# Kernel optimization log

Hardware: AMD Instinct MI355X
Metric: run time of the kernel (lower is better)

## Reference

```python
import jax, jax.numpy as jnp
import numpy as np

D_MODEL = 1024
N_HEADS = 16
D_K = D_MODEL // N_HEADS


def _glorot(key, fan_in, fan_out):
    limit = np.sqrt(6.0 / (fan_in + fan_out)).astype(np.float32)
    return jax.random.uniform(key, (fan_in, fan_out), jnp.float32, -limit, limit)


def setup_inputs() -> dict:
    key = jax.random.key(0)
    kx, kq, kk, kv = jax.random.split(key, 4)
    x = jax.random.normal(kx, (2, 2048, D_MODEL), jnp.float32)
    Wq = _glorot(kq, D_MODEL, D_MODEL)
    Wk = _glorot(kk, D_MODEL, D_MODEL)
    Wv = _glorot(kv, D_MODEL, D_MODEL)
    bq = jnp.zeros((D_MODEL,), jnp.float32)
    bk = jnp.zeros((D_MODEL,), jnp.float32)
    bv = jnp.zeros((D_MODEL,), jnp.float32)
    return {"x": x, "Wq": Wq, "bq": bq, "Wk": Wk, "bk": bk, "Wv": Wv, "bv": bv}


def reference(x, Wq, bq, Wk, bk, Wv, bv):
    B, S, _ = x.shape
    # QKV projections (Dense layers with bias)
    q = (x @ Wq + bq).reshape(B, S, N_HEADS, D_K).transpose(0, 2, 1, 3)  # [B,H,S,Dk]
    k = (x @ Wk + bk).reshape(B, S, N_HEADS, D_K).transpose(0, 2, 1, 3)
    v = (x @ Wv + bv).reshape(B, S, N_HEADS, D_K).transpose(0, 2, 1, 3)
    # raw exp-based softmax (NO max subtraction, per original module)
    scores = jnp.einsum('bhqd,bhkd->bhqk', q, k) / np.sqrt(D_K).astype(np.float32)
    scores = jnp.exp(scores)
    attn = scores / (jnp.sum(scores, axis=-1, keepdims=True) + 1e-8)
    context = jnp.einsum('bhqk,bhkd->bhqd', attn, v)  # [B,H,S,Dk]
    return context.transpose(0, 2, 1, 3).reshape(B, S, N_HEADS * D_K)
```

## Files before the change

### kernel.cpp

```cpp
#include <hip/hip_runtime.h>
#include <hip/hip_bf16.h>
#include <stdint.h>

typedef __bf16 bf16x8 __attribute__((ext_vector_type(8)));
typedef __bf16 bf16x4 __attribute__((ext_vector_type(4)));
typedef float  f32x4  __attribute__((ext_vector_type(4)));
typedef unsigned short u16_t;

#define MFMA(a, b, c) __builtin_amdgcn_mfma_f32_16x16x32_bf16((a), (b), (c), 0, 0, 0)

__device__ __forceinline__ void cp16(const void* g, void* l) {
  __builtin_amdgcn_global_load_lds(
      (const __attribute__((address_space(1))) unsigned int*)g,
      (__attribute__((address_space(3))) unsigned int*)l, 16, 0, 0);
}

__device__ __forceinline__ unsigned pkbf(float a, float b) {
  __bf16 x = (__bf16)a, y = (__bf16)b;
  return ((unsigned)*(u16_t*)&y << 16) | (unsigned)*(u16_t*)&x;
}

__global__ __launch_bounds__(256) void k_cvt_x(const float* __restrict__ in,
                                               u16_t* __restrict__ out, int n4) {
  int i = blockIdx.x * 256 + threadIdx.x;
  if (i >= n4) return;
  float4 f = ((const float4*)in)[i];
  bf16x4 o = {(__bf16)f.x, (__bf16)f.y, (__bf16)f.z, (__bf16)f.w};
  *(bf16x4*)&out[(size_t)i * 4] = o;
}

__global__ __launch_bounds__(256) void k_cvt_w(const float* __restrict__ W0,
                                               const float* __restrict__ W1,
                                               const float* __restrict__ W2,
                                               u16_t* __restrict__ Wt) {
  __shared__ u16_t T[64][65];
  const float* W = blockIdx.z == 0 ? W0 : (blockIdx.z == 1 ? W1 : W2);
  int k0 = blockIdx.y * 64, n0 = blockIdx.x * 64;
  int t = threadIdx.x;
#pragma unroll
  for (int i = 0; i < 16; i++) {
    int e = i * 256 + t, r = e >> 6, c = e & 63;
    __bf16 hv = (__bf16)W[(size_t)(k0 + r) * 1024 + n0 + c];
    T[r][c] = *(u16_t*)&hv;
  }
  __syncthreads();
  size_t base = ((size_t)blockIdx.z * 1024 + n0) * 1024 + k0;
#pragma unroll
  for (int i = 0; i < 16; i++) {
    int e = i * 256 + t, r = e >> 6, c = e & 63;
    Wt[base + (size_t)r * 1024 + c] = T[c][r];
  }
}

__global__ __launch_bounds__(256) void k_gemm_qkv(
    const u16_t* __restrict__ A, const u16_t* __restrict__ Bt,
    const float* __restrict__ bq, const float* __restrict__ bk,
    const float* __restrict__ bv,
    u16_t* __restrict__ Qo, u16_t* __restrict__ Ko, u16_t* __restrict__ Vo) {
  __shared__ u16_t As[128 * 32];
  __shared__ u16_t Bs[128 * 32];
  const int tid = threadIdx.x, lane = tid & 63, wv = tid >> 6;
  const int quad = lane >> 4, col = lane & 15;
  const int wm = wv >> 1, wn = wv & 1;
  const int tn = blockIdx.x * 128, tm = blockIdx.y * 128;
  f32x4 acc[4][4] = {};

  const int c0 = wv * 2;
  const int srow = lane >> 2;
  const int spc = lane & 3;

  for (int kk = 0; kk < 1024; kk += 32) {
#pragma unroll
    for (int i = 0; i < 2; i++) {
      int c = c0 + i;
      int m = c * 16 + srow;
      int lch = spc ^ ((m >> 1) & 3);
      cp16(A + (size_t)(tm + m) * 1024 + kk + lch * 8, As + c * 512 + lane * 8);
      cp16(Bt + (size_t)(tn + m) * 1024 + kk + lch * 8, Bs + c * 512 + lane * 8);
    }
    __syncthreads();
    bf16x8 af[4], bfv[4];
#pragma unroll
    for (int mt = 0; mt < 4; mt++) {
      int row = wm * 64 + mt * 16 + col;
      af[mt] = *(const bf16x8*)&As[row * 32 + (quad ^ ((row >> 1) & 3)) * 8];
    }
#pragma unroll
    for (int nt = 0; nt < 4; nt++) {
      int row = wn * 64 + nt * 16 + col;
      bfv[nt] = *(const bf16x8*)&Bs[row * 32 + (quad ^ ((row >> 1) & 3)) * 8];
    }
#pragma unroll
    for (int mt = 0; mt < 4; mt++)
#pragma unroll
      for (int nt = 0; nt < 4; nt++)
        acc[mt][nt] = MFMA(af[mt], bfv[nt], acc[mt][nt]);
    __syncthreads();
  }

  const int mat = tn >> 10;
  const float* bias = mat == 0 ? bq : (mat == 1 ? bk : bv);
  if (mat == 2) {
#pragma unroll
    for (int nt = 0; nt < 4; nt++) {
      int gn = tn + wn * 64 + nt * 16 + col;
      int d = gn & 1023, h = d >> 6, dk = d & 63;
      float bb = bias[d];
#pragma unroll
      for (int mt = 0; mt < 4; mt++) {
        int gm = tm + wm * 64 + mt * 16 + quad * 4;
        int b = gm >> 11, s = gm & 2047;
        bf16x4 pk4;
#pragma unroll
        for (int r = 0; r < 4; r++) pk4[r] = (__bf16)(acc[mt][nt][r] + bb);
        *(bf16x4*)&Vo[((size_t)((b * 16 + h) * 64 + dk)) * 2048 + s] = pk4;
      }
    }
  } else {
    u16_t* O = mat == 0 ? Qo : Ko;
    const float scl = mat == 0 ? 0.18033688011112042f : 1.0f;
#pragma unroll
    for (int nt = 0; nt < 4; nt++) {
      int gn = tn + wn * 64 + nt * 16 + col;
      int d = gn & 1023, h = d >> 6, dk = d & 63;
      float bb = bias[d];
#pragma unroll
      for (int mt = 0; mt < 4; mt++) {
#pragma unroll
        for (int r = 0; r < 4; r++) {
          int gm = tm + wm * 64 + mt * 16 + quad * 4 + r;
          int b = gm >> 11, s = gm & 2047;
          __bf16 hv = (__bf16)((acc[mt][nt][r] + bb) * scl);
          O[((size_t)((b * 16 + h) * 2048 + s)) * 64 + dk] = *(u16_t*)&hv;
        }
      }
    }
  }
}

__global__ __launch_bounds__(128, 2) void k_attn(const u16_t* __restrict__ Q,
                                                 const u16_t* __restrict__ K,
                                                 const u16_t* __restrict__ Vt,
                                                 float* __restrict__ out) {
  __shared__ u16_t smem[20480];
  u16_t* Qs  = smem;
  u16_t* Ksb = smem + 4096;
  u16_t* Vsb = smem + 12288;
  const int tid = threadIdx.x, lane = tid & 63, wk = tid >> 6;
  const int quad = lane >> 4, col = lane & 15;
  const int qt = blockIdx.x, bh = blockIdx.y;
  const int b = bh >> 4, h = bh & 15;
  const int r8 = lane >> 3, c8 = lane & 7;

  const u16_t* Qg = Q + ((size_t)bh * 2048 + qt * 64) * 64;
  const u16_t* Kg = K + (size_t)bh * 2048 * 64;
  const u16_t* Vg = Vt + (size_t)bh * 64 * 2048;

#pragma unroll
  for (int i = 0; i < 4; i++) {
    int c = wk * 4 + i;
    int row = c * 8 + r8;
    int lch = c8 ^ (row & 7);
    cp16(Qg + (size_t)row * 64 + lch * 8, Qs + c * 512 + lane * 8);
    cp16(Kg + (size_t)row * 64 + lch * 8, Ksb + c * 512 + lane * 8);
    cp16(Vg + (size_t)row * 2048 + lch * 8, Vsb + c * 512 + lane * 8);
  }
  __syncthreads();

  bf16x8 qf[4][2];
#pragma unroll
  for (int nt = 0; nt < 4; nt++)
#pragma unroll
    for (int ks = 0; ks < 2; ks++) {
      int row = nt * 16 + col;
      qf[nt][ks] = *(const bf16x8*)&Qs[row * 64 + (((ks * 4 + quad) ^ (row & 7)) * 8)];
    }
  __syncthreads();

  u16_t* Pw = Qs + wk * 2048;

  bf16x8 ones;
#pragma unroll
  for (int j = 0; j < 8; j++) ones[j] = (__bf16)1.0f;

  f32x4 ao[4][4] = {};
  f32x4 dn[4] = {};

  for (int kt = 0; kt < 32; kt++) {
    const int cur = kt & 1;
    const u16_t* Kc = Ksb + cur * 4096;
    const u16_t* Vc = Vsb + cur * 4096;
    if (kt + 1 < 32) {
      u16_t* Kn = Ksb + (cur ^ 1) * 4096;
      u16_t* Vn = Vsb + (cur ^ 1) * 4096;
#pragma unroll
      for (int i = 0; i < 4; i++) {
        int c = wk * 4 + i;
        int row = c * 8 + r8;
        int lch = c8 ^ (row & 7);
        cp16(Kg + (size_t)(kt + 1) * 4096 + (size_t)row * 64 + lch * 8,
             Kn + c * 512 + lane * 8);
        cp16(Vg + (size_t)row * 2048 + (kt + 1) * 64 + lch * 8,
             Vn + c * 512 + lane * 8);
      }
    }

    f32x4 sc[2][4] = {};
#pragma unroll
    for (int ks = 0; ks < 2; ks++) {
      bf16x8 kf[2];
#pragma unroll
      for (int mt = 0; mt < 2; mt++) {
        int row = wk * 32 + mt * 16 + col;
        kf[mt] = *(const bf16x8*)&Kc[row * 64 + (((ks * 4 + quad) ^ (row & 7)) * 8)];
      }
#pragma unroll
      for (int mt = 0; mt < 2; mt++)
#pragma unroll
        for (int nt = 0; nt < 4; nt++)
          sc[mt][nt] = MFMA(kf[mt], qf[nt][ks], sc[mt][nt]);
    }

#pragma unroll
    for (int mt = 0; mt < 2; mt++)
#pragma unroll
      for (int nt = 0; nt < 4; nt++) {
        int ql = nt * 16 + col;
        unsigned lo = pkbf(__builtin_amdgcn_exp2f(sc[mt][nt][0]),
                           __builtin_amdgcn_exp2f(sc[mt][nt][1]));
        unsigned hi = pkbf(__builtin_amdgcn_exp2f(sc[mt][nt][2]),
                           __builtin_amdgcn_exp2f(sc[mt][nt][3]));
        int kp = (mt * 16 + quad * 4) ^ (((ql >> 1) & 3) << 3);
        *(uint2*)&Pw[ql * 32 + kp] = make_uint2(lo, hi);
      }

    bf16x8 vf[4];
#pragma unroll
    for (int dt = 0; dt < 4; dt++) {
      int row = dt * 16 + col;
      vf[dt] = *(const bf16x8*)&Vc[row * 64 + (((wk * 4 + quad) ^ (row & 7)) * 8)];
    }

#pragma unroll
    for (int nt = 0; nt < 4; nt++) {
      int ql = nt * 16 + col;
      bf16x8 pf = *(const bf16x8*)&Pw[ql * 32 + ((quad * 8) ^ (((ql >> 1) & 3) << 3))];
      dn[nt] = MFMA(pf, ones, dn[nt]);
#pragma unroll
      for (int dt = 0; dt < 4; dt++)
        ao[nt][dt] = MFMA(pf, vf[dt], ao[nt][dt]);
    }
    __syncthreads();
  }

  float* red = (float*)(smem + 4096);
  if (wk == 1) {
#pragma unroll
    for (int nt = 0; nt < 4; nt++) {
#pragma unroll
      for (int dt = 0; dt < 4; dt++)
#pragma unroll
        for (int r = 0; r < 4; r++)
          red[lane * 81 + (nt * 4 + dt) * 4 + r] = ao[nt][dt][r];
#pragma unroll
      for (int r = 0; r < 4; r++)
        red[lane * 81 + 64 + nt * 4 + r] = dn[nt][r];
    }
  }
  __syncthreads();
  if (wk == 0) {
#pragma unroll
    for (int nt = 0; nt < 4; nt++) {
      float dsum[4];
#pragma unroll
      for (int r = 0; r < 4; r++)
        dsum[r] = dn[nt][r] + red[lane * 81 + 64 + nt * 4 + r] + 1e-8f;
#pragma unroll
      for (int dt = 0; dt < 4; dt++) {
#pragma unroll
        for (int r = 0; r < 4; r++) {
          float v = (ao[nt][dt][r] + red[lane * 81 + (nt * 4 + dt) * 4 + r]) / dsum[r];
          int s = qt * 64 + nt * 16 + quad * 4 + r;
          out[((size_t)b * 2048 + s) * 1024 + h * 64 + dt * 16 + col] = v;
        }
      }
    }
  }
}

extern "C" void kernel_launch(void* const* d_in, const int* in_sizes, int n_in,
                              void* d_out, int out_size, void* d_ws, size_t ws_size,
                              hipStream_t stream) {
  const float* x  = (const float*)d_in[0];
  const float* Wq = (const float*)d_in[1];
  const float* bq = (const float*)d_in[2];
  const float* Wk = (const float*)d_in[3];
  const float* bk = (const float*)d_in[4];
  const float* Wv = (const float*)d_in[5];
  const float* bv = (const float*)d_in[6];
  float* out = (float*)d_out;

  char* ws = (char*)d_ws;
  u16_t* xb  = (u16_t*)(ws);
  u16_t* Wt  = (u16_t*)(ws + 8388608);
  u16_t* Qb  = (u16_t*)(ws + 14680064);
  u16_t* Kb  = (u16_t*)(ws + 23068672);
  u16_t* Vtb = (u16_t*)(ws + 31457280);

  hipLaunchKernelGGL(k_cvt_x, dim3(4096), dim3(256), 0, stream, x, xb, 1048576);
  hipLaunchKernelGGL(k_cvt_w, dim3(16, 16, 3), dim3(256), 0, stream, Wq, Wk, Wv, Wt);
  hipLaunchKernelGGL(k_gemm_qkv, dim3(24, 32), dim3(256), 0, stream,
                     xb, Wt, bq, bk, bv, Qb, Kb, Vtb);
  hipLaunchKernelGGL(k_attn, dim3(32, 32), dim3(128), 0, stream, Qb, Kb, Vtb, out);
}
```

Baseline: 172.1 us.

## Split attention block into four waves over query and key halves; merge prep kernels

The attention kernel moves from 2 waves to 4 waves per block. Each wave now handles half the query rows and half of each key tile, and the P-tile layout and the cross-wave reduction are adapted to match. The intent is to cut per-wave register pressure and raise occupancy and latency hiding. The x conversion and weight transpose kernels are fused into one launch to save a kernel launch. In exchange there is more LDS traffic and synchronization per block, with more waves contending for the same shared tiles.

```diff
diff --git a/kernel.cpp b/kernel.cpp
--- a/kernel.cpp
+++ b/kernel.cpp
@@ -20,23 +20,25 @@
   return ((unsigned)*(u16_t*)&y << 16) | (unsigned)*(u16_t*)&x;
 }
 
-__global__ __launch_bounds__(256) void k_cvt_x(const float* __restrict__ in,
-                                               u16_t* __restrict__ out, int n4) {
-  int i = blockIdx.x * 256 + threadIdx.x;
-  if (i >= n4) return;
-  float4 f = ((const float4*)in)[i];
-  bf16x4 o = {(__bf16)f.x, (__bf16)f.y, (__bf16)f.z, (__bf16)f.w};
-  *(bf16x4*)&out[(size_t)i * 4] = o;
-}
-
-__global__ __launch_bounds__(256) void k_cvt_w(const float* __restrict__ W0,
-                                               const float* __restrict__ W1,
-                                               const float* __restrict__ W2,
-                                               u16_t* __restrict__ Wt) {
+__global__ __launch_bounds__(256) void k_prep(const float* __restrict__ x,
+                                              const float* __restrict__ W0,
+                                              const float* __restrict__ W1,
+                                              const float* __restrict__ W2,
+                                              u16_t* __restrict__ xb,
+                                              u16_t* __restrict__ Wt) {
   __shared__ u16_t T[64][65];
-  const float* W = blockIdx.z == 0 ? W0 : (blockIdx.z == 1 ? W1 : W2);
-  int k0 = blockIdx.y * 64, n0 = blockIdx.x * 64;
-  int t = threadIdx.x;
+  int bx = blockIdx.x, t = threadIdx.x;
+  if (bx < 4096) {
+    int i = bx * 256 + t;
+    float4 f = ((const float4*)x)[i];
+    bf16x4 o = {(__bf16)f.x, (__bf16)f.y, (__bf16)f.z, (__bf16)f.w};
+    *(bf16x4*)&xb[(size_t)i * 4] = o;
+    return;
+  }
+  int j = bx - 4096;
+  int nx = j & 15, ny = (j >> 4) & 15, z = j >> 8;
+  const float* W = z == 0 ? W0 : (z == 1 ? W1 : W2);
+  int k0 = ny * 64, n0 = nx * 64;
 #pragma unroll
   for (int i = 0; i < 16; i++) {
     int e = i * 256 + t, r = e >> 6, c = e & 63;
@@ -44,7 +46,7 @@
     T[r][c] = *(u16_t*)&hv;
   }
   __syncthreads();
-  size_t base = ((size_t)blockIdx.z * 1024 + n0) * 1024 + k0;
+  size_t base = ((size_t)z * 1024 + n0) * 1024 + k0;
 #pragma unroll
   for (int i = 0; i < 16; i++) {
     int e = i * 256 + t, r = e >> 6, c = e & 63;
@@ -138,7 +140,7 @@
   }
 }
 
-__global__ __launch_bounds__(128, 2) void k_attn(const u16_t* __restrict__ Q,
+__global__ __launch_bounds__(256, 4) void k_attn(const u16_t* __restrict__ Q,
                                                  const u16_t* __restrict__ K,
                                                  const u16_t* __restrict__ Vt,
                                                  float* __restrict__ out) {
@@ -146,8 +148,9 @@
   u16_t* Qs  = smem;
   u16_t* Ksb = smem + 4096;
   u16_t* Vsb = smem + 12288;
-  const int tid = threadIdx.x, lane = tid & 63, wk = tid >> 6;
+  const int tid = threadIdx.x, lane = tid & 63, wv = tid >> 6;
   const int quad = lane >> 4, col = lane & 15;
+  const int qh = wv >> 1, kh = wv & 1;
   const int qt = blockIdx.x, bh = blockIdx.y;
   const int b = bh >> 4, h = bh & 15;
   const int r8 = lane >> 3, c8 = lane & 7;
@@ -157,34 +160,35 @@
   const u16_t* Vg = Vt + (size_t)bh * 64 * 2048;
 
 #pragma unroll
-  for (int i = 0; i < 4; i++) {
-    int c = wk * 4 + i;
+  for (int i = 0; i < 2; i++) {
+    int c = wv * 2 + i;
     int row = c * 8 + r8;
-    int lch = c8 ^ (row & 7);
+    int lch = c8 ^ r8;
     cp16(Qg + (size_t)row * 64 + lch * 8, Qs + c * 512 + lane * 8);
     cp16(Kg + (size_t)row * 64 + lch * 8, Ksb + c * 512 + lane * 8);
     cp16(Vg + (size_t)row * 2048 + lch * 8, Vsb + c * 512 + lane * 8);
   }
   __syncthreads();
 
-  bf16x8 qf[4][2];
-#pragma unroll
-  for (int nt = 0; nt < 4; nt++)
+  bf16x8 qf[2][2];
+#pragma unroll
+  for (int nt = 0; nt < 2; nt++)
 #pragma unroll
     for (int ks = 0; ks < 2; ks++) {
-      int row = nt * 16 + col;
+      int row = qh * 32 + nt * 16 + col;
       qf[nt][ks] = *(const bf16x8*)&Qs[row * 64 + (((ks * 4 + quad) ^ (row & 7)) * 8)];
     }
   __syncthreads();
 
-  u16_t* Pw = Qs + wk * 2048;
+  u16_t* Pq = Qs + qh * 2048;
+  const int gcol = ((col >> 1) & 3) << 2;
 
   bf16x8 ones;
 #pragma unroll
   for (int j = 0; j < 8; j++) ones[j] = (__bf16)1.0f;
 
-  f32x4 ao[4][4] = {};
-  f32x4 dn[4] = {};
+  f32x4 ao[2][4] = {};
+  f32x4 dn[2] = {};
 
   for (int kt = 0; kt < 32; kt++) {
     const int cur = kt & 1;
@@ -194,10 +198,10 @@
       u16_t* Kn = Ksb + (cur ^ 1) * 4096;
       u16_t* Vn = Vsb + (cur ^ 1) * 4096;
 #pragma unroll
-      for (int i = 0; i < 4; i++) {
-        int c = wk * 4 + i;
+      for (int i = 0; i < 2; i++) {
+        int c = wv * 2 + i;
         int row = c * 8 + r8;
-        int lch = c8 ^ (row & 7);
+        int lch = c8 ^ r8;
         cp16(Kg + (size_t)(kt + 1) * 4096 + (size_t)row * 64 + lch * 8,
              Kn + c * 512 + lane * 8);
         cp16(Vg + (size_t)row * 2048 + (kt + 1) * 64 + lch * 8,
@@ -205,46 +209,47 @@
       }
     }
 
-    f32x4 sc[2][4] = {};
+    f32x4 sc[2][2] = {};
 #pragma unroll
     for (int ks = 0; ks < 2; ks++) {
       bf16x8 kf[2];
 #pragma unroll
       for (int mt = 0; mt < 2; mt++) {
-        int row = wk * 32 + mt * 16 + col;
+        int row = kh * 32 + mt * 16 + col;
         kf[mt] = *(const bf16x8*)&Kc[row * 64 + (((ks * 4 + quad) ^ (row & 7)) * 8)];
       }
 #pragma unroll
       for (int mt = 0; mt < 2; mt++)
 #pragma unroll
-        for (int nt = 0; nt < 4; nt++)
+        for (int nt = 0; nt < 2; nt++)
           sc[mt][nt] = MFMA(kf[mt], qf[nt][ks], sc[mt][nt]);
     }
 
 #pragma unroll
     for (int mt = 0; mt < 2; mt++)
 #pragma unroll
-      for (int nt = 0; nt < 4; nt++) {
-        int ql = nt * 16 + col;
+      for (int nt = 0; nt < 2; nt++) {
+        int q = nt * 16 + col;
         unsigned lo = pkbf(__builtin_amdgcn_exp2f(sc[mt][nt][0]),
                            __builtin_amdgcn_exp2f(sc[mt][nt][1]));
         unsigned hi = pkbf(__builtin_amdgcn_exp2f(sc[mt][nt][2]),
                            __builtin_amdgcn_exp2f(sc[mt][nt][3]));
-        int kp = (mt * 16 + quad * 4) ^ (((ql >> 1) & 3) << 3);
-        *(uint2*)&Pw[ql * 32 + kp] = make_uint2(lo, hi);
+        int slot = (kh * 8 + mt * 4 + quad) ^ gcol;
+        *(uint2*)&Pq[q * 64 + slot * 4] = make_uint2(lo, hi);
       }
 
     bf16x8 vf[4];
 #pragma unroll
     for (int dt = 0; dt < 4; dt++) {
       int row = dt * 16 + col;
-      vf[dt] = *(const bf16x8*)&Vc[row * 64 + (((wk * 4 + quad) ^ (row & 7)) * 8)];
-    }
-
-#pragma unroll
-    for (int nt = 0; nt < 4; nt++) {
-      int ql = nt * 16 + col;
-      bf16x8 pf = *(const bf16x8*)&Pw[ql * 32 + ((quad * 8) ^ (((ql >> 1) & 3) << 3))];
+      vf[dt] = *(const bf16x8*)&Vc[row * 64 + (((kh * 4 + quad) ^ (row & 7)) * 8)];
+    }
+
+#pragma unroll
+    for (int nt = 0; nt < 2; nt++) {
+      int q = nt * 16 + col;
+      int slot = (kh * 8 + 2 * quad) ^ gcol;
+      bf16x8 pf = *(const bf16x8*)&Pq[q * 64 + slot * 4];
       dn[nt] = MFMA(pf, ones, dn[nt]);
 #pragma unroll
       for (int dt = 0; dt < 4; dt++)
@@ -254,33 +259,34 @@
   }
 
   float* red = (float*)(smem + 4096);
-  if (wk == 1) {
-#pragma unroll
-    for (int nt = 0; nt < 4; nt++) {
+  const int rb = (qh * 64 + lane) * 41;
+  if (kh == 1) {
+#pragma unroll
+    for (int nt = 0; nt < 2; nt++) {
 #pragma unroll
       for (int dt = 0; dt < 4; dt++)
 #pragma unroll
         for (int r = 0; r < 4; r++)
-          red[lane * 81 + (nt * 4 + dt) * 4 + r] = ao[nt][dt][r];
+          red[rb + (nt * 4 + dt) * 4 + r] = ao[nt][dt][r];
 #pragma unroll
       for (int r = 0; r < 4; r++)
-        red[lane * 81 + 64 + nt * 4 + r] = dn[nt][r];
+        red[rb + 32 + nt * 4 + r] = dn[nt][r];
     }
   }
   __syncthreads();
-  if (wk == 0) {
-#pragma unroll
-    for (int nt = 0; nt < 4; nt++) {
+  if (kh == 0) {
+#pragma unroll
+    for (int nt = 0; nt < 2; nt++) {
       float dsum[4];
 #pragma unroll
       for (int r = 0; r < 4; r++)
-        dsum[r] = dn[nt][r] + red[lane * 81 + 64 + nt * 4 + r] + 1e-8f;
+        dsum[r] = dn[nt][r] + red[rb + 32 + nt * 4 + r] + 1e-8f;
 #pragma unroll
       for (int dt = 0; dt < 4; dt++) {
 #pragma unroll
         for (int r = 0; r < 4; r++) {
-          float v = (ao[nt][dt][r] + red[lane * 81 + (nt * 4 + dt) * 4 + r]) / dsum[r];
-          int s = qt * 64 + nt * 16 + quad * 4 + r;
+          float v = (ao[nt][dt][r] + red[rb + (nt * 4 + dt) * 4 + r]) / dsum[r];
+          int s = qt * 64 + qh * 32 + nt * 16 + quad * 4 + r;
           out[((size_t)b * 2048 + s) * 1024 + h * 64 + dt * 16 + col] = v;
         }
       }
@@ -307,9 +313,8 @@
   u16_t* Kb  = (u16_t*)(ws + 23068672);
   u16_t* Vtb = (u16_t*)(ws + 31457280);
 
-  hipLaunchKernelGGL(k_cvt_x, dim3(4096), dim3(256), 0, stream, x, xb, 1048576);
-  hipLaunchKernelGGL(k_cvt_w, dim3(16, 16, 3), dim3(256), 0, stream, Wq, Wk, Wv, Wt);
+  hipLaunchKernelGGL(k_prep, dim3(4864), dim3(256), 0, stream, x, Wq, Wk, Wv, xb, Wt);
   hipLaunchKernelGGL(k_gemm_qkv, dim3(24, 32), dim3(256), 0, stream,
                      xb, Wt, bq, bk, bv, Qb, Kb, Vtb);
-  hipLaunchKernelGGL(k_attn, dim3(32, 32), dim3(128), 0, stream, Qb, Kb, Vtb, out);
-}
+  hipLaunchKernelGGL(k_attn, dim3(32, 32), dim3(256), 0, stream, Qb, Kb, Vtb, out);
+}
```

Result: no change. 174.7 us (+1.5%).
